# Performance work log

Measured on AMD Instinct MI355X. Metric: run time of the kernel, lower is better.

Reference implementation:

```python
import jax, jax.numpy as jnp
import numpy as np

N_NODES = 50000
N_EDGES = 160000
D = 512
N_GRAPHS = 64
EPS = 1e-5


def setup_inputs() -> dict:
    key = jax.random.key(0)
    ks = jax.random.split(key, 8)
    node = jax.random.normal(ks[0], (N_NODES, D), dtype=jnp.float32)
    edge_index = jax.random.randint(ks[1], (2, N_EDGES), 0, N_NODES, dtype=jnp.int64)
    edge_attr = jax.random.uniform(ks[2], (N_EDGES,), dtype=jnp.float32)
    batch_ptr = jnp.sort(jax.random.randint(ks[3], (N_NODES,), 0, N_GRAPHS, dtype=jnp.int64))
    W = jax.random.normal(ks[4], (D, D), dtype=jnp.float32) / np.float32(np.sqrt(D))
    b = jnp.zeros((D,), dtype=jnp.float32)
    gn_weight = jnp.ones((D,), dtype=jnp.float32)
    gn_bias = jnp.zeros((D,), dtype=jnp.float32)
    gn_mean_scale = jnp.ones((D,), dtype=jnp.float32)
    return {"node": node, "edge_attr": edge_attr, "W": W, "b": b,
            "gn_weight": gn_weight, "gn_bias": gn_bias, "gn_mean_scale": gn_mean_scale,
            "edge_index": edge_index, "batch_ptr": batch_ptr}


def _gcn_conv(x, edge_index, edge_weight, W, b):
    # x: [N, D]. PyG GCNConv(normalize=True): lin -> add self-loops -> D^-1/2 A D^-1/2 -> + bias
    x = x @ W  # [N, D]
    loop = jnp.arange(N_NODES, dtype=edge_index.dtype)
    row = jnp.concatenate([edge_index[0], loop])  # source
    col = jnp.concatenate([edge_index[1], loop])  # target
    w = jnp.concatenate([edge_weight, jnp.ones((N_NODES,), dtype=x.dtype)])
    deg = jax.ops.segment_sum(w, col, num_segments=N_NODES)  # weighted in-degree incl. self-loop
    dis = jnp.where(deg > 0, jax.lax.rsqrt(deg), 0.0)
    norm = dis[row] * w * dis[col]  # [E+N]
    msgs = x[row] * norm[:, None]  # gather + scale
    out = jax.ops.segment_sum(msgs, col, num_segments=N_NODES)  # scatter-add
    return out + b


def _graph_norm(x, batch, weight, bias, mean_scale):
    # PyG GraphNorm: per-graph mean/var over nodes, learnable mean scale alpha
    ones = jnp.ones((x.shape[0],), dtype=x.dtype)
    count = jax.ops.segment_sum(ones, batch, num_segments=N_GRAPHS)  # [G]
    count = jnp.maximum(count, 1.0)[:, None]
    mean = jax.ops.segment_sum(x, batch, num_segments=N_GRAPHS) / count  # [G, D]
    centered = x - mean[batch] * mean_scale  # [N, D]
    var = jax.ops.segment_sum(centered * centered, batch, num_segments=N_GRAPHS) / count
    inv_std = jax.lax.rsqrt(var + EPS)  # [G, D]
    return weight * centered * inv_std[batch] + bias


def reference(node, edge_attr, W, b, gn_weight, gn_bias, gn_mean_scale, edge_index, batch_ptr):
    conv = _gcn_conv(node, edge_index, edge_attr, W, b)
    h = node + conv  # skip_connection=True
    h = _graph_norm(h, batch_ptr, gn_weight, gn_bias, gn_mean_scale)
    return jax.nn.relu(h)
```

## Files before the change

### kernel.cpp

```cpp
#include <hip/hip_runtime.h>


#define N_NODES 50000
#define PADN    50048
#define N_EDGES 160000
#define DIM 512
#define N_GRAPHS 64
#define EPSV 1e-5f
#define CAP 32

#define ZWORDS (2 * N_NODES + 2 * N_GRAPHS * DIM + N_GRAPHS)

typedef short short8 __attribute__((ext_vector_type(8)));
typedef float floatx4 __attribute__((ext_vector_type(4)));

#define FENCE() do { asm volatile("" ::: "memory"); __builtin_amdgcn_sched_barrier(0); } while (0)

__device__ __forceinline__ unsigned short f2bf(float x) {
    unsigned int u = __float_as_uint(x);
    u += 0x7FFFu + ((u >> 16) & 1u);
    return (unsigned short)(u >> 16);
}
__device__ __forceinline__ float bf2f(unsigned short s) {
    return __uint_as_float(((unsigned int)s) << 16);
}
__device__ __forceinline__ float bflo(int p) {
    return __uint_as_float(((unsigned int)p) << 16);
}
__device__ __forceinline__ float bfhi(int p) {
    return __uint_as_float(((unsigned int)p) & 0xFFFF0000u);
}
__device__ __forceinline__ int pkbf(float lo, float hi) {
    int r;
    asm("v_cvt_pk_bf16_f32 %0, %1, %2" : "=v"(r) : "v"(lo), "v"(hi));
    return r;
}

__global__ __launch_bounds__(256) void k_zero(int* __restrict__ z) {
    int i = (blockIdx.x * 256 + threadIdx.x) * 4;
    if (i < ZWORDS) {
        int4 zz = make_int4(0, 0, 0, 0);
        *(int4*)&z[i] = zz;
    }
}

__global__ __launch_bounds__(256) void k_prep(const float* __restrict__ W,
                                              short* __restrict__ Wt,
                                              const int* __restrict__ ei,
                                              const float* __restrict__ ew,
                                              float* __restrict__ degsum,
                                              int* __restrict__ cursor,
                                              int* __restrict__ srcs,
                                              float* __restrict__ wts) {
    int t = threadIdx.x;
    {
        int i = blockIdx.x * 256 + t;
        int k = i >> 9, n = i & 511;
        Wt[n * 512 + k] = (short)f2bf(W[i]);
    }
    if (blockIdx.x < 625) {
        int e = blockIdx.x * 256 + t;
        int r = ei[e];
        int c = ei[N_EDGES + e];
        float w = ew[e];
        atomicAdd(&degsum[c], w);
        int pos = atomicAdd(&cursor[c], 1);
        if (pos < CAP) {
            srcs[(size_t)c * CAP + pos] = r;
            wts[(size_t)c * CAP + pos] = w;
        }
    }
}

__global__ __launch_bounds__(256) void k_gemm_mfma(const float* __restrict__ Af,
                                                   const short* __restrict__ Bt,
                                                   short* __restrict__ Cbf) {
    __shared__ short As[2][128 * 64];
    __shared__ short Bs[128 * 64];
    const int tid  = threadIdx.x;
    const int wave = tid >> 6;
    const int lane = tid & 63;
    const int l16  = lane & 15;
    const int quad = lane >> 4;
    const int row0 = blockIdx.y * 128;
    const int col0 = blockIdx.x * 128;
    const int mb = (wave >> 1) * 64;
    const int nb = (wave & 1) * 64;

    floatx4 acc[4][4];
    const floatx4 z = {0.f, 0.f, 0.f, 0.f};
#pragma unroll
    for (int i = 0; i < 4; ++i)
#pragma unroll
        for (int j = 0; j < 4; ++j) acc[i][j] = z;

    const int srow = lane >> 3;
    const int scol = ((lane & 7) ^ srow) * 8;

    float4 av0[4], av1[4];

#define LOAD_A_REGS(kk)                                                                   \
    _Pragma("unroll")                                                                     \
    for (int j = 0; j < 4; ++j) {                                                         \
        int grow = row0 + wave * 32 + j * 8 + srow;                                       \
        if (grow > N_NODES - 1) grow = N_NODES - 1;         \
        const float* src = Af + (size_t)grow * DIM + (kk) + scol;                         \
        av0[j] = *(const float4*)src;                                                     \
        av1[j] = *(const float4*)(src + 4);                                               \
    }
#define WRITE_A_LDS(buf)                                                                  \
    _Pragma("unroll")                                                                     \
    for (int j = 0; j < 4; ++j) {                                                         \
        int4 o;                                                                           \
        o.x = pkbf(av0[j].x, av0[j].y);                                                   \
        o.y = pkbf(av0[j].z, av0[j].w);                                                   \
        o.z = pkbf(av1[j].x, av1[j].y);                                                   \
        o.w = pkbf(av1[j].z, av1[j].w);                                                   \
        *(int4*)&As[buf][(wave * 4 + j) * 512 + lane * 8] = o;                            \
    }
#define STAGE_B(kk)                                                                       \
    _Pragma("unroll")                                                                     \
    for (int j = 0; j < 4; ++j) {                                                         \
        int seg = wave * 4 + j;                                                           \
        int r = seg * 8 + srow;                                                           \
        __builtin_amdgcn_global_load_lds(                                                 \
            (const __attribute__((address_space(1))) void*)(Bt + (size_t)(col0 + r) * DIM + (kk) + scol),  \
            (__attribute__((address_space(3))) void*)(Bs + seg * 512 + lane * 8),         \
            16, 0, 0);                                                                    \
    }

    LOAD_A_REGS(0);
    int cur = 0;
#pragma unroll 1
    for (int t = 0; t < 8; ++t) {
        const int kk = t * 64;
        STAGE_B(kk);
        FENCE();
        WRITE_A_LDS(cur);
        FENCE();
        if (t < 7) {
            LOAD_A_REGS(kk + 64);
            FENCE();
            asm volatile("s_waitcnt vmcnt(8) lgkmcnt(0)" ::: "memory");
        } else {
            asm volatile("s_waitcnt vmcnt(0) lgkmcnt(0)" ::: "memory");
        }
        __builtin_amdgcn_s_barrier();
        FENCE();
#pragma unroll
        for (int kh = 0; kh < 2; ++kh) {
            short8 af[4], bfr[4];
#pragma unroll
            for (int i = 0; i < 4; ++i) {
                int rr = mb + i * 16 + l16;
                int ck = (kh * 4 + quad) ^ (rr & 7);
                af[i] = *(const short8*)&As[cur][rr * 64 + ck * 8];
            }
#pragma unroll
            for (int j = 0; j < 4; ++j) {
                int rb = nb + j * 16 + l16;
                int ck = (kh * 4 + quad) ^ (rb & 7);
                bfr[j] = *(const short8*)&Bs[rb * 64 + ck * 8];
            }
#pragma unroll
            for (int i = 0; i < 4; ++i)
#pragma unroll
                for (int j = 0; j < 4; ++j)
                    acc[i][j] = __builtin_amdgcn_mfma_f32_16x16x32_bf16(bfr[j], af[i], acc[i][j], 0, 0, 0);
        }
        FENCE();
        __builtin_amdgcn_s_barrier();
        cur ^= 1;
    }
#undef LOAD_A_REGS
#undef WRITE_A_LDS
#undef STAGE_B
#pragma unroll
    for (int i = 0; i < 4; ++i) {
        int row = row0 + mb + i * 16 + l16;
#pragma unroll
        for (int j = 0; j < 4; ++j) {
            int col = col0 + nb + j * 16 + quad * 4;
            ushort4 pk;
            pk.x = f2bf(acc[i][j][0]);
            pk.y = f2bf(acc[i][j][1]);
            pk.z = f2bf(acc[i][j][2]);
            pk.w = f2bf(acc[i][j][3]);
            *(ushort4*)&Cbf[(size_t)row * DIM + col] = pk;
        }
    }
}

__global__ __launch_bounds__(256) void k_gather(const int* __restrict__ cursor,
                                                const int* __restrict__ srcs,
                                                const float* __restrict__ wts,
                                                const short* __restrict__ xWb,
                                                const float* __restrict__ node,
                                                short* __restrict__ hbuf,
                                                const float* __restrict__ b,
                                                const float* __restrict__ degsum) {
    const int lane = threadIdx.x & 63;
    const int n = __builtin_amdgcn_readfirstlane(blockIdx.x * 4 + (threadIdx.x >> 6));
    const int q = lane * 8;
    if (n >= N_NODES) {
        int4 zz = make_int4(0, 0, 0, 0);
        *(int4*)&hbuf[(size_t)n * DIM + q] = zz;
        return;
    }
    const float dn = rsqrtf(1.0f + degsum[n]);
    int cnt = cursor[n];
    if (cnt > CAP) cnt = CAP;
    const size_t ebase = (size_t)n * CAP;

    float a0, a1, a2, a3, a4, a5, a6, a7;
    {
        int4 raw = *(const int4*)&xWb[(size_t)n * DIM + q];
        a0 = dn * bflo(raw.x); a1 = dn * bfhi(raw.x);
        a2 = dn * bflo(raw.y); a3 = dn * bfhi(raw.y);
        a4 = dn * bflo(raw.z); a5 = dn * bfhi(raw.z);
        a6 = dn * bflo(raw.w); a7 = dn * bfhi(raw.w);
    }
    for (int i = 0; i < cnt; ++i) {
        int s = srcs[ebase + i];
        float w = wts[ebase + i] * rsqrtf(1.0f + degsum[s]);
        int4 raw = *(const int4*)&xWb[(size_t)s * DIM + q];
        a0 = fmaf(w, bflo(raw.x), a0); a1 = fmaf(w, bfhi(raw.x), a1);
        a2 = fmaf(w, bflo(raw.y), a2); a3 = fmaf(w, bfhi(raw.y), a3);
        a4 = fmaf(w, bflo(raw.z), a4); a5 = fmaf(w, bfhi(raw.z), a5);
        a6 = fmaf(w, bflo(raw.w), a6); a7 = fmaf(w, bfhi(raw.w), a7);
    }
    float4 x0 = *(const float4*)&node[(size_t)n * DIM + q];
    float4 x1 = *(const float4*)&node[(size_t)n * DIM + q + 4];
    float4 b0 = *(const float4*)&b[q];
    float4 b1 = *(const float4*)&b[q + 4];
    float h0 = x0.x + b0.x + dn * a0;
    float h1 = x0.y + b0.y + dn * a1;
    float h2 = x0.z + b0.z + dn * a2;
    float h3 = x0.w + b0.w + dn * a3;
    float h4 = x1.x + b1.x + dn * a4;
    float h5 = x1.y + b1.y + dn * a5;
    float h6 = x1.z + b1.z + dn * a6;
    float h7 = x1.w + b1.w + dn * a7;
    int4 o;
    o.x = ((unsigned)f2bf(h1) << 16) | f2bf(h0);
    o.y = ((unsigned)f2bf(h3) << 16) | f2bf(h2);
    o.z = ((unsigned)f2bf(h5) << 16) | f2bf(h4);
    o.w = ((unsigned)f2bf(h7) << 16) | f2bf(h6);
    *(int4*)&hbuf[(size_t)n * DIM + q] = o;
}

__global__ __launch_bounds__(256) void k_stats(const short* __restrict__ hB,
                                               const int* __restrict__ batch,
                                               float* __restrict__ Sx,
                                               float* __restrict__ Sxx,
                                               float* __restrict__ cntg) {
    const int half = threadIdx.x >> 7;
    const int q = (threadIdx.x & 127) * 4;
    const int lead = (threadIdx.x & 127) == 0;
    const int n0 = blockIdx.x * 64;
    const int g0 = batch[n0];
    int nl = n0 + 63;
    if (nl > N_NODES - 1) nl = N_NODES - 1;
    const int gL = batch[nl];

    if (gL <= g0 + 1) {
        float sxA0 = 0.f, sxA1 = 0.f, sxA2 = 0.f, sxA3 = 0.f;
        float xxA0 = 0.f, xxA1 = 0.f, xxA2 = 0.f, xxA3 = 0.f;
        float sxB0 = 0.f, sxB1 = 0.f, sxB2 = 0.f, sxB3 = 0.f;
        float xxB0 = 0.f, xxB1 = 0.f, xxB2 = 0.f, xxB3 = 0.f;
        float cA = 0.f, cB = 0.f;
#pragma unroll 8
        for (int r = 0; r < 32; ++r) {
            int n = n0 + r * 2 + half;
            int nn = (n < N_NODES) ? n : (N_NODES - 1);
            int g = batch[nn];
            ushort4 hv = *(const ushort4*)&hB[(size_t)n * DIM + q];
            float m = (g == g0) ? 1.f : 0.f;
            float vld = (n < N_NODES) ? 1.f : 0.f;
            float h0 = bf2f(hv.x), h1 = bf2f(hv.y), h2 = bf2f(hv.z), h3 = bf2f(hv.w);
            float a0 = h0 * m, a1 = h1 * m, a2 = h2 * m, a3 = h3 * m;
            sxA0 += a0;            sxA1 += a1;
            sxA2 += a2;            sxA3 += a3;
            xxA0 = fmaf(a0, h0, xxA0); xxA1 = fmaf(a1, h1, xxA1);
            xxA2 = fmaf(a2, h2, xxA2); xxA3 = fmaf(a3, h3, xxA3);
            float b0v = h0 - a0, b1v = h1 - a1, b2v = h2 - a2, b3v = h3 - a3;
            sxB0 += b0v;           sxB1 += b1v;
            sxB2 += b2v;           sxB3 += b3v;
            xxB0 = fmaf(b0v, h0, xxB0); xxB1 = fmaf(b1v, h1, xxB1);
            xxB2 = fmaf(b2v, h2, xxB2); xxB3 = fmaf(b3v, h3, xxB3);
            cA += vld * m;
            cB += vld * (1.f - m);
        }
        atomicAdd(&Sx[g0 * DIM + q + 0], sxA0);
        atomicAdd(&Sx[g0 * DIM + q + 1], sxA1);
        atomicAdd(&Sx[g0 * DIM + q + 2], sxA2);
        atomicAdd(&Sx[g0 * DIM + q + 3], sxA3);
        atomicAdd(&Sxx[g0 * DIM + q + 0], xxA0);
        atomicAdd(&Sxx[g0 * DIM + q + 1], xxA1);
        atomicAdd(&Sxx[g0 * DIM + q + 2], xxA2);
        atomicAdd(&Sxx[g0 * DIM + q + 3], xxA3);
        if (lead) atomicAdd(&cntg[g0], cA);
        if (gL != g0) {
            atomicAdd(&Sx[gL * DIM + q + 0], sxB0);
            atomicAdd(&Sx[gL * DIM + q + 1], sxB1);
            atomicAdd(&Sx[gL * DIM + q + 2], sxB2);
            atomicAdd(&Sx[gL * DIM + q + 3], sxB3);
            atomicAdd(&Sxx[gL * DIM + q + 0], xxB0);
            atomicAdd(&Sxx[gL * DIM + q + 1], xxB1);
            atomicAdd(&Sxx[gL * DIM + q + 2], xxB2);
            atomicAdd(&Sxx[gL * DIM + q + 3], xxB3);
            if (lead) atomicAdd(&cntg[gL], cB);
        }
    } else {
        for (int r = 0; r < 32; ++r) {
            int n = n0 + r * 2 + half;
            if (n >= N_NODES) break;
            int g = batch[n];
            ushort4 hv = *(const ushort4*)&hB[(size_t)n * DIM + q];
            float h0 = bf2f(hv.x), h1 = bf2f(hv.y), h2 = bf2f(hv.z), h3 = bf2f(hv.w);
            atomicAdd(&Sx[g * DIM + q + 0], h0);
            atomicAdd(&Sx[g * DIM + q + 1], h1);
            atomicAdd(&Sx[g * DIM + q + 2], h2);
            atomicAdd(&Sx[g * DIM + q + 3], h3);
            atomicAdd(&Sxx[g * DIM + q + 0], h0 * h0);
            atomicAdd(&Sxx[g * DIM + q + 1], h1 * h1);
            atomicAdd(&Sxx[g * DIM + q + 2], h2 * h2);
            atomicAdd(&Sxx[g * DIM + q + 3], h3 * h3);
            if (lead) atomicAdd(&cntg[g], 1.f);
        }
    }
}

__global__ __launch_bounds__(256) void k_norm(const short* __restrict__ hB,
                                              const int* __restrict__ batch,
                                              const float* __restrict__ Sx,
                                              const float* __restrict__ Sxx,
                                              const float* __restrict__ cntg,
                                              const float* __restrict__ alpha,
                                              const float* __restrict__ gw,
                                              const float* __restrict__ gb,
                                              float* __restrict__ out) {
    size_t idx = (size_t)blockIdx.x * 256 + threadIdx.x;
    int n = (int)(idx >> 7);
    int q = ((int)idx & 127) * 4;
    if (n >= N_NODES) return;
    int g = batch[n];
    float c = fmaxf(cntg[g], 1.0f);
    float rc = __builtin_amdgcn_rcpf(c);
    float4 sx = *(const float4*)&Sx[(size_t)g * DIM + q];
    float4 xx = *(const float4*)&Sxx[(size_t)g * DIM + q];
    float4 al = *(const float4*)&alpha[q];
    float4 w4 = *(const float4*)&gw[q];
    float4 b4 = *(const float4*)&gb[q];
    ushort4 hv = *(const ushort4*)&hB[(size_t)n * DIM + q];
    float m0 = sx.x * rc, m1 = sx.y * rc, m2 = sx.z * rc, m3 = sx.w * rc;
    float ma0 = m0 * al.x, ma1 = m1 * al.y, ma2 = m2 * al.z, ma3 = m3 * al.w;
    float iv0 = rsqrtf(xx.x * rc - 2.f * m0 * ma0 + ma0 * ma0 + EPSV);
    float iv1 = rsqrtf(xx.y * rc - 2.f * m1 * ma1 + ma1 * ma1 + EPSV);
    float iv2 = rsqrtf(xx.z * rc - 2.f * m2 * ma2 + ma2 * ma2 + EPSV);
    float iv3 = rsqrtf(xx.w * rc - 2.f * m3 * ma3 + ma3 * ma3 + EPSV);
    float4 r;
    r.x = fmaxf(0.f, (bf2f(hv.x) - ma0) * iv0 * w4.x + b4.x);
    r.y = fmaxf(0.f, (bf2f(hv.y) - ma1) * iv1 * w4.y + b4.y);
    r.z = fmaxf(0.f, (bf2f(hv.z) - ma2) * iv2 * w4.z + b4.z);
    r.w = fmaxf(0.f, (bf2f(hv.w) - ma3) * iv3 * w4.w + b4.w);
    *(float4*)&out[(size_t)n * DIM + q] = r;
}

extern "C" void kernel_launch(void* const* d_in, const int* in_sizes, int n_in,
                              void* d_out, int out_size, void* d_ws, size_t ws_size,
                              hipStream_t stream) {
    const float* node  = (const float*)d_in[0];
    const float* eattr = (const float*)d_in[1];
    const float* W     = (const float*)d_in[2];
    const float* b     = (const float*)d_in[3];
    const float* gw    = (const float*)d_in[4];
    const float* gb    = (const float*)d_in[5];
    const float* alpha = (const float*)d_in[6];
    const int*   ei    = (const int*)d_in[7];
    const int*   batch = (const int*)d_in[8];
    float* out = (float*)d_out;

    short* hbuf   = (short*)d_ws;
    short* xWb    = hbuf + (size_t)PADN * DIM;
    short* Wt     = xWb + (size_t)PADN * DIM;
    float* degsum = (float*)(Wt + DIM * DIM);
    int*   cursor = (int*)(degsum + N_NODES);
    float* Sx     = (float*)(cursor + N_NODES);
    float* Sxx    = Sx + N_GRAPHS * DIM;
    float* cntg   = Sxx + N_GRAPHS * DIM;
    float* wts    = cntg + N_GRAPHS;
    int*   srcs   = (int*)(wts + (size_t)N_NODES * CAP);

    k_zero<<<(ZWORDS / 4 + 255) / 256, 256, 0, stream>>>((int*)degsum);
    k_prep<<<1024, 256, 0, stream>>>(W, Wt, ei, eattr, degsum, cursor, srcs, wts);
    dim3 ggrid(4, PADN / 128);
    k_gemm_mfma<<<ggrid, 256, 0, stream>>>(node, Wt, xWb);
    k_gather<<<PADN / 4, 256, 0, stream>>>(cursor, srcs, wts, xWb, node, hbuf, b, degsum);
    k_stats<<<(N_NODES + 63) / 64, 256, 0, stream>>>(hbuf, batch, Sx, Sxx, cntg);
    k_norm<<<25000, 256, 0, stream>>>(hbuf, batch, Sx, Sxx, cntg, alpha, gw, gb, out);
}
```

Before: 375.7 us.

## Shrink GEMM tile to 128x64, double-buffer B, prefetch A two stages ahead

The GEMM tile goes from 128x128 to 128x64 output per block. B now has two LDS buffers, and A is prefetched two k-steps ahead through two register sets, so the next B stage and A loads overlap with the current MFMA work. Blocks are remapped so that the 8 column tiles of one row panel sit close together in launch order, which should help L2 reuse of A, and launch_bounds asks for 4 blocks per CU. The aim is more concurrent blocks and better latency hiding. The cost is that each fp32 A row panel is now loaded and converted twice, once per column half, and the extra prefetch registers add register pressure.

Result: slower. 394.8 us (+5.1%).

```diff
diff --git a/kernel.cpp b/kernel.cpp
--- a/kernel.cpp
+++ b/kernel.cpp
@@ -72,76 +72,84 @@
     }
 }
 
-__global__ __launch_bounds__(256) void k_gemm_mfma(const float* __restrict__ Af,
-                                                   const short* __restrict__ Bt,
-                                                   short* __restrict__ Cbf) {
+__global__ __launch_bounds__(256, 4) void k_gemm_mfma(const float* __restrict__ Af,
+                                                      const short* __restrict__ Bt,
+                                                      short* __restrict__ Cbf) {
     __shared__ short As[2][128 * 64];
-    __shared__ short Bs[128 * 64];
+    __shared__ short Bs[2][64 * 64];
+    const int panel = blockIdx.x * 49 + (blockIdx.y >> 3);
+    if (panel >= 391) return;
+    const int row0 = panel * 128;
+    const int col0 = (blockIdx.y & 7) * 64;
+
     const int tid  = threadIdx.x;
     const int wave = tid >> 6;
     const int lane = tid & 63;
     const int l16  = lane & 15;
     const int quad = lane >> 4;
-    const int row0 = blockIdx.y * 128;
-    const int col0 = blockIdx.x * 128;
     const int mb = (wave >> 1) * 64;
-    const int nb = (wave & 1) * 64;
-
-    floatx4 acc[4][4];
+    const int nb = (wave & 1) * 32;
+
+    floatx4 acc[4][2];
     const floatx4 z = {0.f, 0.f, 0.f, 0.f};
 #pragma unroll
     for (int i = 0; i < 4; ++i)
 #pragma unroll
-        for (int j = 0; j < 4; ++j) acc[i][j] = z;
+        for (int j = 0; j < 2; ++j) acc[i][j] = z;
 
     const int srow = lane >> 3;
     const int scol = ((lane & 7) ^ srow) * 8;
 
-    float4 av0[4], av1[4];
-
-#define LOAD_A_REGS(kk)                                                                   \
+    float4 a0v0[4], a0v1[4];
+    float4 a1v0[4], a1v1[4];
+
+#define LOAD_A_REGS(S, kk)                                                                \
     _Pragma("unroll")                                                                     \
     for (int j = 0; j < 4; ++j) {                                                         \
         int grow = row0 + wave * 32 + j * 8 + srow;                                       \
         if (grow > N_NODES - 1) grow = N_NODES - 1;         \
         const float* src = Af + (size_t)grow * DIM + (kk) + scol;                         \
-        av0[j] = *(const float4*)src;                                                     \
-        av1[j] = *(const float4*)(src + 4);                                               \
-    }
-#define WRITE_A_LDS(buf)                                                                  \
+        a##S##v0[j] = *(const float4*)src;                                                \
+        a##S##v1[j] = *(const float4*)(src + 4);                                          \
+    }
+#define WRITE_A_LDS(S, buf)                                                               \
     _Pragma("unroll")                                                                     \
     for (int j = 0; j < 4; ++j) {                                                         \
         int4 o;                                                                           \
-        o.x = pkbf(av0[j].x, av0[j].y);                                                   \
-        o.y = pkbf(av0[j].z, av0[j].w);                                                   \
-        o.z = pkbf(av1[j].x, av1[j].y);                                                   \
-        o.w = pkbf(av1[j].z, av1[j].w);                                                   \
+        o.x = pkbf(a##S##v0[j].x, a##S##v0[j].y);                                         \
+        o.y = pkbf(a##S##v0[j].z, a##S##v0[j].w);                                         \
+        o.z = pkbf(a##S##v1[j].x, a##S##v1[j].y);                                         \
+        o.w = pkbf(a##S##v1[j].z, a##S##v1[j].w);                                         \
         *(int4*)&As[buf][(wave * 4 + j) * 512 + lane * 8] = o;                            \
     }
-#define STAGE_B(kk)                                                                       \
+#define STAGE_B(buf, kk)                                                                  \
     _Pragma("unroll")                                                                     \
-    for (int j = 0; j < 4; ++j) {                                                         \
-        int seg = wave * 4 + j;                                                           \
-        int r = seg * 8 + srow;                                                           \
+    for (int j = 0; j < 2; ++j) {                                                         \
+        int seg = wave * 2 + j;                                                           \
+        int r = seg * 8 + srow;                                            \
         __builtin_amdgcn_global_load_lds(                                                 \
             (const __attribute__((address_space(1))) void*)(Bt + (size_t)(col0 + r) * DIM + (kk) + scol),  \
-            (__attribute__((address_space(3))) void*)(Bs + seg * 512 + lane * 8),         \
+            (__attribute__((address_space(3))) void*)(&Bs[buf][0] + seg * 512 + lane * 8),\
             16, 0, 0);                                                                    \
     }
 
-    LOAD_A_REGS(0);
-    int cur = 0;
+    LOAD_A_REGS(0, 0);
+    STAGE_B(0, 0);
+    LOAD_A_REGS(1, 64);
+    FENCE();
 #pragma unroll 1
     for (int t = 0; t < 8; ++t) {
-        const int kk = t * 64;
-        STAGE_B(kk);
+        const int p = t & 1;
+        if (p == 0) { WRITE_A_LDS(0, 0); } else { WRITE_A_LDS(1, 1); }
         FENCE();
-        WRITE_A_LDS(cur);
-        FENCE();
+        if (t < 7) { STAGE_B(p ^ 1, (t + 1) * 64); FENCE(); }
+        if (t < 6) {
+            if (p == 0) { LOAD_A_REGS(0, (t + 2) * 64); }
+            else        { LOAD_A_REGS(1, (t + 2) * 64); }
+            FENCE();
+        }
         if (t < 7) {
-            LOAD_A_REGS(kk + 64);
-            FENCE();
-            asm volatile("s_waitcnt vmcnt(8) lgkmcnt(0)" ::: "memory");
+            asm volatile("s_waitcnt vmcnt(10) lgkmcnt(0)" ::: "memory");
         } else {
             asm volatile("s_waitcnt vmcnt(0) lgkmcnt(0)" ::: "memory");
         }
@@ -149,28 +157,27 @@
         FENCE();
 #pragma unroll
         for (int kh = 0; kh < 2; ++kh) {
-            short8 af[4], bfr[4];
+            short8 af[4], bfr[2];
 #pragma unroll
             for (int i = 0; i < 4; ++i) {
                 int rr = mb + i * 16 + l16;
                 int ck = (kh * 4 + quad) ^ (rr & 7);
-                af[i] = *(const short8*)&As[cur][rr * 64 + ck * 8];
+                af[i] = *(const short8*)&As[p][rr * 64 + ck * 8];
             }
 #pragma unroll
-            for (int j = 0; j < 4; ++j) {
+            for (int j = 0; j < 2; ++j) {
                 int rb = nb + j * 16 + l16;
                 int ck = (kh * 4 + quad) ^ (rb & 7);
-                bfr[j] = *(const short8*)&Bs[rb * 64 + ck * 8];
+                bfr[j] = *(const short8*)&Bs[p][rb * 64 + ck * 8];
             }
 #pragma unroll
             for (int i = 0; i < 4; ++i)
 #pragma unroll
-                for (int j = 0; j < 4; ++j)
+                for (int j = 0; j < 2; ++j)
                     acc[i][j] = __builtin_amdgcn_mfma_f32_16x16x32_bf16(bfr[j], af[i], acc[i][j], 0, 0, 0);
         }
         FENCE();
         __builtin_amdgcn_s_barrier();
-        cur ^= 1;
     }
 #undef LOAD_A_REGS
 #undef WRITE_A_LDS
@@ -179,7 +186,7 @@
     for (int i = 0; i < 4; ++i) {
         int row = row0 + mb + i * 16 + l16;
 #pragma unroll
-        for (int j = 0; j < 4; ++j) {
+        for (int j = 0; j < 2; ++j) {
             int col = col0 + nb + j * 16 + quad * 4;
             ushort4 pk;
             pk.x = f2bf(acc[i][j][0]);
@@ -394,7 +401,7 @@
 
     k_zero<<<(ZWORDS / 4 + 255) / 256, 256, 0, stream>>>((int*)degsum);
     k_prep<<<1024, 256, 0, stream>>>(W, Wt, ei, eattr, degsum, cursor, srcs, wts);
-    dim3 ggrid(4, PADN / 128);
+    dim3 ggrid(8, 392);
     k_gemm_mfma<<<ggrid, 256, 0, stream>>>(node, Wt, xWb);
     k_gather<<<PADN / 4, 256, 0, stream>>>(cursor, srcs, wts, xWb, node, hbuf, b, degsum);
     k_stats<<<(N_NODES + 63) / 64, 256, 0, stream>>>(hbuf, batch, Sx, Sxx, cntg);
```
